# Kernel optimization log

Hardware: AMD Instinct MI355X
Metric: run time of the kernel (lower is better)

Reference implementation:

```python
import jax, jax.numpy as jnp
import numpy as np

NUM_CODES = 512
CODE_DIM = 64
COMMITMENT_COST = 0.1
DECAY = 0.9
EPS = 1e-5


def setup_inputs() -> dict:
    key = jax.random.key(0)
    k1, k2, k3 = jax.random.split(key, 3)
    B, L, D, K = 32, 4096, CODE_DIM, NUM_CODES
    z_e = jax.random.normal(k1, (B, L, D), dtype=jnp.float32)
    emb = jax.random.uniform(k2, (K, D), dtype=jnp.float32, minval=-1.0 / K, maxval=1.0 / K)
    ema_cluster_size = jnp.ones((K,), dtype=jnp.float32)
    ema_w = emb + 0.01 * jax.random.normal(k3, (K, D), dtype=jnp.float32)
    return {"z_e": z_e, "emb": emb, "ema_cluster_size": ema_cluster_size, "ema_w": ema_w}


def reference(z_e, emb, ema_cluster_size, ema_w):
    B, L, D = z_e.shape
    K = emb.shape[0]
    flat = z_e.reshape(-1, D)                                   # [N, D]
    dists = (jnp.sum(flat * flat, axis=1, keepdims=True)
             - 2.0 * flat @ emb.T
             + jnp.sum(emb * emb, axis=1)[None, :])
    codes = jnp.argmin(dists, axis=1)                           # [N] int
    z_q = emb[codes].reshape(B, L, D)
    # straight-through estimator
    z_q_st = z_e + jax.lax.stop_gradient(z_q - z_e)
    # EMA updates (training, no_grad) via direct scatter-reduce instead of one-hot matmul
    cluster_size = jax.ops.segment_sum(jnp.ones_like(codes, dtype=z_e.dtype), codes, num_segments=K)
    new_ecs = ema_cluster_size * DECAY + cluster_size * (1.0 - DECAY)
    dw = jax.ops.segment_sum(flat, codes, num_segments=K)       # [K, D]
    new_ema_w = ema_w * DECAY + dw * (1.0 - DECAY)
    n = jnp.sum(new_ecs)
    cs_smoothed = (new_ecs + EPS) / (n + K * EPS) * n
    new_emb = new_ema_w / (cs_smoothed[:, None] + EPS)
    # commitment loss (z_q detached)
    commit = jnp.mean((z_e - jax.lax.stop_gradient(z_q)) ** 2)
    loss_vq = COMMITMENT_COST * commit
    return (z_q_st, loss_vq, codes.reshape(B, L), new_ecs, new_ema_w, new_emb)
```

## Files before the change

### kernel.cpp

```cpp
#include <hip/hip_runtime.h>
#include <math.h>

#define NROWS 131072
#define DIM 64
#define NCODE 512
#define FLAG_CAP 131072

#define OUT_ZQ    0
#define OUT_LOSS  8388608
#define OUT_CODES 8388609
#define OUT_ECS   8519681
#define OUT_EMAW  8520193
#define OUT_EMB   8552961

#define WS_LOSS    0
#define WS_N       8
#define WS_FLAGC   12
#define WS_COUNTS  16
#define WS_OFFSETS 2064
#define WS_CURSOR  4112
#define WS_CSUM    6160
#define WS_EHI     8208
#define WS_ELO     73744
#define WS_CODESI  139280
#define WS_DW4     139280
#define WS_BUCKET  663568
#define WS_FLAGR   663568
#define WS_BYTES   1187856

#define DECAY_C ((float)0.9)
#define OMD_C   ((float)(1.0 - 0.9))
#define EPS_C   ((float)1e-5)

typedef float f32x4 __attribute__((ext_vector_type(4)));
typedef short short8v __attribute__((ext_vector_type(8)));

__device__ __forceinline__ unsigned short bf16_rne_bits(float f) {
    unsigned int u = __float_as_uint(f);
    unsigned int r = u + 0x7fffu + ((u >> 16) & 1u);
    return (unsigned short)(r >> 16);
}

__device__ __forceinline__ float np_pairwise64_sq(const float* v) {
    float r[8];
#pragma unroll
    for (int j = 0; j < 8; ++j) r[j] = __fmul_rn(v[j], v[j]);
#pragma unroll
    for (int b = 1; b < 8; ++b) {
#pragma unroll
        for (int j = 0; j < 8; ++j)
            r[j] = __fadd_rn(r[j], __fmul_rn(v[8 * b + j], v[8 * b + j]));
    }
    return __fadd_rn(__fadd_rn(__fadd_rn(r[0], r[1]), __fadd_rn(r[2], r[3])),
                     __fadd_rn(__fadd_rn(r[4], r[5]), __fadd_rn(r[6], r[7])));
}

__global__ void k_csum(const float* __restrict__ emb, float* __restrict__ csum,
                       unsigned short* __restrict__ ehi, unsigned short* __restrict__ elo,
                       int* __restrict__ counts, int* __restrict__ flagC,
                       double* __restrict__ lossAcc, float* __restrict__ n_out) {
    int k = blockIdx.x * blockDim.x + threadIdx.x;
    if (k >= NCODE) return;
    counts[k] = 0;
    if (k == 0) { *flagC = 0; *lossAcc = 0.0; *n_out = 0.f; }
    float e[DIM];
#pragma unroll
    for (int d = 0; d < DIM; d += 4) {
        float4 v = *reinterpret_cast<const float4*>(emb + (size_t)k * DIM + d);
        e[d] = v.x; e[d + 1] = v.y; e[d + 2] = v.z; e[d + 3] = v.w;
    }
    csum[k] = np_pairwise64_sq(e);
#pragma unroll
    for (int d = 0; d < DIM; ++d) {
        unsigned short hb = bf16_rne_bits(e[d]);
        float hf = __uint_as_float((unsigned int)hb << 16);
        ehi[k * DIM + d] = hb;
        elo[k * DIM + d] = bf16_rne_bits(e[d] - hf);
    }
}

#define CVTE(H, L, j, val) { \
    unsigned int ub = __float_as_uint(val); \
    unsigned int rr = ub + 0x7fffu + ((ub >> 16) & 1u); \
    unsigned short hb = (unsigned short)(rr >> 16); \
    float hf2 = __uint_as_float(((unsigned int)hb) << 16); \
    float lof = (val) - hf2; \
    unsigned int ul = __float_as_uint(lof); \
    unsigned int rl = ul + 0x7fffu + ((ul >> 16) & 1u); \
    H[j] = (short)hb; L[j] = (short)(rl >> 16); }

__global__ __launch_bounds__(256, 1) void k_mfma(
        const float* __restrict__ ze, const float* __restrict__ emb,
        const unsigned short* __restrict__ ehi, const unsigned short* __restrict__ elo,
        const float* __restrict__ csum, float* __restrict__ out,
        int* __restrict__ codes_i, int* __restrict__ counts,
        double* __restrict__ lossAcc, int* __restrict__ flagC, int* __restrict__ flagR) {
    __shared__ float cs[NCODE];
    __shared__ int h[NCODE];
    __shared__ float A_s[128];
    __shared__ int code_s[128];
    __shared__ double ls[4];
    int tid = threadIdx.x;
    for (int i = tid; i < NCODE; i += 256) { cs[i] = csum[i]; h[i] = 0; }
    if (tid < 128) {
        const float* xr = ze + (size_t)(blockIdx.x * 128 + tid) * DIM;
        float xv[DIM];
#pragma unroll
        for (int d = 0; d < DIM; d += 4) {
            float4 v = *reinterpret_cast<const float4*>(xr + d);
            xv[d] = v.x; xv[d + 1] = v.y; xv[d + 2] = v.z; xv[d + 3] = v.w;
        }
        A_s[tid] = np_pairwise64_sq(xv);
    }
    __syncthreads();

    int wid = tid >> 6;
    int lane = tid & 63;
    int r16 = lane & 15;
    int kg = lane >> 4;
    int rowbase = blockIdx.x * 128 + wid * 32;

    float Ar[2][4];
#pragma unroll
    for (int rt = 0; rt < 2; ++rt)
#pragma unroll
        for (int reg = 0; reg < 4; ++reg)
            Ar[rt][reg] = A_s[wid * 32 + rt * 16 + 4 * kg + reg];

    short8v ahi[2][2], alo[2][2];
#define LOADA(rt, hf) { \
        const float4* ap = reinterpret_cast<const float4*>( \
            ze + (size_t)(rowbase + (rt) * 16 + r16) * DIM + (hf) * 32 + 8 * kg); \
        float4 u = ap[0], w = ap[1]; \
        CVTE(ahi[rt][hf], alo[rt][hf], 0, u.x) CVTE(ahi[rt][hf], alo[rt][hf], 1, u.y) \
        CVTE(ahi[rt][hf], alo[rt][hf], 2, u.z) CVTE(ahi[rt][hf], alo[rt][hf], 3, u.w) \
        CVTE(ahi[rt][hf], alo[rt][hf], 4, w.x) CVTE(ahi[rt][hf], alo[rt][hf], 5, w.y) \
        CVTE(ahi[rt][hf], alo[rt][hf], 6, w.z) CVTE(ahi[rt][hf], alo[rt][hf], 7, w.w) }
    LOADA(0, 0) LOADA(0, 1) LOADA(1, 0) LOADA(1, 1)

    float m1v[2][4], m2v[2][4];
    int i1v[2][4];
#pragma unroll
    for (int rt = 0; rt < 2; ++rt)
#pragma unroll
        for (int j = 0; j < 4; ++j) { m1v[rt][j] = 3.4e38f; m2v[rt][j] = 3.4e38f; i1v[rt][j] = 0; }

#define UPD(C, rt, reg) { \
        float u = __fsub_rn(Ar[rt][reg], __fadd_rn(C[reg], C[reg])); \
        float s = __fadd_rn(u, csv); \
        if (s < m1v[rt][reg]) { m2v[rt][reg] = m1v[rt][reg]; m1v[rt][reg] = s; i1v[rt][reg] = codeIdx; } \
        else if (s < m2v[rt][reg]) { m2v[rt][reg] = s; } }

    for (int t = 0; t < 32; ++t) {
        const short8v* bh = reinterpret_cast<const short8v*>(
            ehi + (size_t)(t * 16 + r16) * DIM + 8 * kg);
        const short8v* bl = reinterpret_cast<const short8v*>(
            elo + (size_t)(t * 16 + r16) * DIM + 8 * kg);
        short8v bh0 = bh[0], bh1 = bh[4];
        short8v bl0 = bl[0], bl1 = bl[4];
        f32x4 c0 = {0.f, 0.f, 0.f, 0.f};
        f32x4 c1 = {0.f, 0.f, 0.f, 0.f};
        c0 = __builtin_amdgcn_mfma_f32_16x16x32_bf16(ahi[0][0], bh0, c0, 0, 0, 0);
        c0 = __builtin_amdgcn_mfma_f32_16x16x32_bf16(ahi[0][1], bh1, c0, 0, 0, 0);
        c0 = __builtin_amdgcn_mfma_f32_16x16x32_bf16(alo[0][0], bh0, c0, 0, 0, 0);
        c0 = __builtin_amdgcn_mfma_f32_16x16x32_bf16(alo[0][1], bh1, c0, 0, 0, 0);
        c0 = __builtin_amdgcn_mfma_f32_16x16x32_bf16(ahi[0][0], bl0, c0, 0, 0, 0);
        c0 = __builtin_amdgcn_mfma_f32_16x16x32_bf16(ahi[0][1], bl1, c0, 0, 0, 0);
        c1 = __builtin_amdgcn_mfma_f32_16x16x32_bf16(ahi[1][0], bh0, c1, 0, 0, 0);
        c1 = __builtin_amdgcn_mfma_f32_16x16x32_bf16(ahi[1][1], bh1, c1, 0, 0, 0);
        c1 = __builtin_amdgcn_mfma_f32_16x16x32_bf16(alo[1][0], bh0, c1, 0, 0, 0);
        c1 = __builtin_amdgcn_mfma_f32_16x16x32_bf16(alo[1][1], bh1, c1, 0, 0, 0);
        c1 = __builtin_amdgcn_mfma_f32_16x16x32_bf16(ahi[1][0], bl0, c1, 0, 0, 0);
        c1 = __builtin_amdgcn_mfma_f32_16x16x32_bf16(ahi[1][1], bl1, c1, 0, 0, 0);
        float csv = cs[t * 16 + r16];
        int codeIdx = t * 16 + r16;
        UPD(c0, 0, 0) UPD(c0, 0, 1) UPD(c0, 0, 2) UPD(c0, 0, 3)
        UPD(c1, 1, 0) UPD(c1, 1, 1) UPD(c1, 1, 2) UPD(c1, 1, 3)
    }

#define RED(rt, reg, mask) { \
        float om1 = __shfl_xor(m1v[rt][reg], mask); \
        int   oi  = __shfl_xor(i1v[rt][reg], mask); \
        float om2 = __shfl_xor(m2v[rt][reg], mask); \
        if (om1 < m1v[rt][reg]) { \
            m2v[rt][reg] = fminf(m1v[rt][reg], om2); m1v[rt][reg] = om1; i1v[rt][reg] = oi; \
        } else if (om1 > m1v[rt][reg]) { \
            m2v[rt][reg] = fminf(m2v[rt][reg], om1); \
        } else { \
            if (oi < i1v[rt][reg]) i1v[rt][reg] = oi; \
            m2v[rt][reg] = m1v[rt][reg]; } }
#define RED4(rt, reg) RED(rt, reg, 1) RED(rt, reg, 2) RED(rt, reg, 4) RED(rt, reg, 8)
    RED4(0, 0) RED4(0, 1) RED4(0, 2) RED4(0, 3)
    RED4(1, 0) RED4(1, 1) RED4(1, 2) RED4(1, 3)

    if (r16 == 0) {
#define WOUT(rt, reg) { \
        int lrow = wid * 32 + (rt) * 16 + 4 * kg + (reg); \
        int row = blockIdx.x * 128 + lrow; \
        code_s[lrow] = i1v[rt][reg]; \
        out[OUT_CODES + row] = (float)i1v[rt][reg]; \
        codes_i[row] = i1v[rt][reg]; \
        atomicAdd(&h[i1v[rt][reg]], 1); \
        if (m2v[rt][reg] - m1v[rt][reg] < Ar[rt][reg] * 3e-7f) { \
            int pos = atomicAdd(flagC, 1); \
            if (pos < FLAG_CAP) flagR[pos] = row; } }
        WOUT(0, 0) WOUT(0, 1) WOUT(0, 2) WOUT(0, 3)
        WOUT(1, 0) WOUT(1, 1) WOUT(1, 2) WOUT(1, 3)
    }
    __syncthreads();

    double lpart = 0.0;
#pragma unroll 4
    for (int r = 0; r < 32; ++r) {
        int code = code_s[wid * 32 + r];
        int row = rowbase + r;
        float x = ze[(size_t)row * DIM + lane];
        float e = emb[(size_t)code * DIM + lane];
        float tdiff = __fsub_rn(e, x);
        out[OUT_ZQ + (size_t)row * DIM + lane] = __fadd_rn(x, tdiff);
        lpart += (double)tdiff * tdiff;
    }
    for (int off = 32; off; off >>= 1) lpart += __shfl_down(lpart, off);
    if (lane == 0) ls[wid] = lpart;
    __syncthreads();
    if (tid == 0) atomicAdd(lossAcc, (ls[0] + ls[1]) + (ls[2] + ls[3]));
    for (int k = tid; k < NCODE; k += 256) {
        int cc = h[k];
        if (cc) atomicAdd(&counts[k], cc);
    }
}

__global__ __launch_bounds__(256) void k_rescue(
        const float* __restrict__ ze, const float* __restrict__ emb,
        const float* __restrict__ csum, float* __restrict__ out,
        int* __restrict__ codes_i, int* __restrict__ counts,
        double* __restrict__ lossAcc, const int* __restrict__ flagC,
        const int* __restrict__ flagR) {
    __shared__ float xs[4][DIM];
    int nf = *flagC;
    if (nf > FLAG_CAP) nf = FLAG_CAP;
    int w = threadIdx.x >> 6;
    int lane = threadIdx.x & 63;
    for (int i = blockIdx.x * 4 + w; i < nf; i += gridDim.x * 4) {
        int row = flagR[i];
        float v = ze[(size_t)row * DIM + lane];
        xs[w][lane] = __fadd_rn(v, v);
        __builtin_amdgcn_wave_barrier();
        float r[8];
#pragma unroll
        for (int j = 0; j < 8; ++j) r[j] = __fmul_rn(xs[w][j], xs[w][j]);
#pragma unroll
        for (int b = 1; b < 8; ++b) {
#pragma unroll
            for (int j = 0; j < 8; ++j)
                r[j] = __fadd_rn(r[j], __fmul_rn(xs[w][8 * b + j], xs[w][8 * b + j]));
        }
        float A = __fmul_rn(0.25f,
            __fadd_rn(__fadd_rn(__fadd_rn(r[0], r[1]), __fadd_rn(r[2], r[3])),
                      __fadd_rn(__fadd_rn(r[4], r[5]), __fadd_rn(r[6], r[7]))));
        float m1 = 3.4e38f;
        int i1 = 0x7fffffff;
#pragma unroll
        for (int kk = 0; kk < 8; ++kk) {
            int k = lane * 8 + kk;
            const float4* e4 = reinterpret_cast<const float4*>(emb + (size_t)k * DIM);
            float a = 0.f;
#pragma unroll
            for (int j = 0; j < 16; ++j) {
                float4 ev = e4[j];
                a = __builtin_fmaf(xs[w][4 * j + 0], ev.x, a);
                a = __builtin_fmaf(xs[w][4 * j + 1], ev.y, a);
                a = __builtin_fmaf(xs[w][4 * j + 2], ev.z, a);
                a = __builtin_fmaf(xs[w][4 * j + 3], ev.w, a);
            }
            float t = __fadd_rn(__fsub_rn(A, a), csum[k]);
            if (t < m1) { m1 = t; i1 = k; }
        }
        for (int off = 32; off; off >>= 1) {
            float ov = __shfl_xor(m1, off);
            int oi = __shfl_xor(i1, off);
            if (ov < m1 || (ov == m1 && oi < i1)) { m1 = ov; i1 = oi; }
        }
        int oldc = codes_i[row];
        if (i1 != oldc) {
            if (lane == 0) {
                codes_i[row] = i1;
                out[OUT_CODES + row] = (float)i1;
                atomicSub(&counts[oldc], 1);
                atomicAdd(&counts[i1], 1);
            }
            float x = __fmul_rn(0.5f, xs[w][lane]);
            float en = emb[(size_t)i1 * DIM + lane];
            float eo = emb[(size_t)oldc * DIM + lane];
            float tn = __fsub_rn(en, x);
            float to = __fsub_rn(eo, x);
            out[OUT_ZQ + (size_t)row * DIM + lane] = __fadd_rn(x, tn);
            double dl = (double)tn * tn - (double)to * to;
            for (int off = 32; off; off >>= 1) dl += __shfl_down(dl, off);
            if (lane == 0) atomicAdd(lossAcc, dl);
        }
        __builtin_amdgcn_wave_barrier();
    }
}

__global__ __launch_bounds__(512) void k_scan(
        const int* __restrict__ counts, int* __restrict__ offsets, int* __restrict__ cursor,
        const float* __restrict__ ecs_in, float* __restrict__ out, float* __restrict__ n_out) {
    __shared__ int sa[NCODE], sb[NCODE];
    __shared__ float red[NCODE];
    int k = threadIdx.x;
    int c = counts[k];
    sa[k] = c;
    float v = __fadd_rn(__fmul_rn(ecs_in[k], DECAY_C), __fmul_rn((float)c, OMD_C));
    out[OUT_ECS + k] = v;
    red[k] = v;
    __syncthreads();
    int* src = sa;
    int* dst = sb;
    for (int off = 1; off < NCODE; off <<= 1) {
        dst[k] = (k >= off) ? src[k - off] + src[k] : src[k];
        __syncthreads();
        int* tp = src; src = dst; dst = tp;
    }
    offsets[k] = src[k] - c;
    cursor[k]  = src[k] - c;
    for (int s = NCODE / 2; s > 0; s >>= 1) {
        if (k < s) red[k] += red[k + s];
        __syncthreads();
    }
    if (k == 0) n_out[0] = red[0];
}

__global__ __launch_bounds__(256) void k_scatter(
        const int* __restrict__ codes_i, int* __restrict__ cursor, int* __restrict__ bucket) {
    int row = blockIdx.x * 256 + threadIdx.x;
    int c = codes_i[row];
    int pos = atomicAdd(&cursor[c], 1);
    bucket[pos] = row;
}

__global__ __launch_bounds__(256) void k_dw(
        const float* __restrict__ ze, const int* __restrict__ bucket,
        const int* __restrict__ offsets, const int* __restrict__ counts,
        float* __restrict__ dw4) {
    __shared__ float p[4][DIM];
    int k = blockIdx.x >> 2;
    int q = blockIdx.x & 3;
    int w = threadIdx.x >> 6;
    int d = threadIdx.x & 63;
    int s = offsets[k];
    int n = counts[k];
    float acc0 = 0.f, acc1 = 0.f;
    int i = q + 4 * w;
    for (; i + 16 < n; i += 32) {
        int ra = bucket[s + i];
        int rb = bucket[s + i + 16];
        acc0 += ze[(size_t)ra * DIM + d];
        acc1 += ze[(size_t)rb * DIM + d];
    }
    if (i < n) acc0 += ze[(size_t)bucket[s + i] * DIM + d];
    p[w][d] = acc0 + acc1;
    __syncthreads();
    if (w == 0) dw4[((size_t)q * NCODE + k) * DIM + d] = (p[0][d] + p[1][d]) + (p[2][d] + p[3][d]);
}

__global__ __launch_bounds__(256) void k_final(
        const float* __restrict__ ema_w, const float* __restrict__ dw4,
        const float* __restrict__ n_ptr, const double* __restrict__ lossAcc,
        float* __restrict__ out) {
    int i = blockIdx.x * blockDim.x + threadIdx.x;
    if (i >= NCODE * DIM) return;
    int k = i >> 6;
    float dsum = __fadd_rn(__fadd_rn(dw4[i], dw4[i + NCODE * DIM]),
                           __fadd_rn(dw4[i + 2 * NCODE * DIM], dw4[i + 3 * NCODE * DIM]));
    float w = __fadd_rn(__fmul_rn(ema_w[i], DECAY_C), __fmul_rn(dsum, OMD_C));
    out[OUT_EMAW + i] = w;
    float n = n_ptr[0];
    float necs = out[OUT_ECS + k];
    float cs = (necs + EPS_C) / (n + (float)NCODE * EPS_C) * n;
    out[OUT_EMB + i] = w / (cs + EPS_C);
    if (i == 0) out[OUT_LOSS] = (float)(0.1 * (lossAcc[0] / (double)((size_t)NROWS * DIM)));
}

extern "C" void kernel_launch(void* const* d_in, const int* in_sizes, int n_in,
                              void* d_out, int out_size, void* d_ws, size_t ws_size,
                              hipStream_t stream) {
    const float* ze   = (const float*)d_in[0];
    const float* emb  = (const float*)d_in[1];
    const float* ecs  = (const float*)d_in[2];
    const float* emaw = (const float*)d_in[3];
    float* out = (float*)d_out;
    char* ws = (char*)d_ws;
    double* lossAcc = (double*)(ws + WS_LOSS);
    float*  n_out   = (float*)(ws + WS_N);
    int*    flagC   = (int*)(ws + WS_FLAGC);
    int*    counts  = (int*)(ws + WS_COUNTS);
    int*    offsets = (int*)(ws + WS_OFFSETS);
    int*    cursor  = (int*)(ws + WS_CURSOR);
    float*  csum    = (float*)(ws + WS_CSUM);
    unsigned short* ehi = (unsigned short*)(ws + WS_EHI);
    unsigned short* elo = (unsigned short*)(ws + WS_ELO);
    int*    codes_i = (int*)(ws + WS_CODESI);
    float*  dw4     = (float*)(ws + WS_DW4);
    int*    bucket  = (int*)(ws + WS_BUCKET);
    int*    flagR   = (int*)(ws + WS_FLAGR);

    hipLaunchKernelGGL(k_csum, dim3(2), dim3(256), 0, stream,
                       emb, csum, ehi, elo, counts, flagC, lossAcc, n_out);
    hipLaunchKernelGGL(k_mfma, dim3(NROWS / 128), dim3(256), 0, stream,
                       ze, emb, ehi, elo, csum, out, codes_i, counts, lossAcc, flagC, flagR);
    hipLaunchKernelGGL(k_rescue, dim3(1024), dim3(256), 0, stream,
                       ze, emb, csum, out, codes_i, counts, lossAcc, flagC, flagR);
    hipLaunchKernelGGL(k_scan, dim3(1), dim3(512), 0, stream,
                       counts, offsets, cursor, ecs, out, n_out);
    hipLaunchKernelGGL(k_scatter, dim3(NROWS / 256), dim3(256), 0, stream,
                       codes_i, cursor, bucket);
    hipLaunchKernelGGL(k_dw, dim3(NCODE * 4), dim3(256), 0, stream,
                       ze, bucket, offsets, counts, dw4);
    hipLaunchKernelGGL(k_final, dim3(NCODE * DIM / 256), dim3(256), 0, stream,
                       emaw, dw4, n_out, lossAcc, out);
}
```

Measured before the change: 208.3 us.

## Split codebook across wave pairs, halve rows per block, merge top-2 via LDS

Result: slower. 225.7 us (+8.4%).

```diff
diff --git a/kernel.cpp b/kernel.cpp
--- a/kernel.cpp
+++ b/kernel.cpp
@@ -97,13 +97,15 @@
         double* __restrict__ lossAcc, int* __restrict__ flagC, int* __restrict__ flagR) {
     __shared__ float cs[NCODE];
     __shared__ int h[NCODE];
-    __shared__ float A_s[128];
-    __shared__ int code_s[128];
+    __shared__ float A_s[64];
+    __shared__ int code_s[64];
+    __shared__ float ms1[64], ms2[64];
+    __shared__ int mi[64];
     __shared__ double ls[4];
     int tid = threadIdx.x;
     for (int i = tid; i < NCODE; i += 256) { cs[i] = csum[i]; h[i] = 0; }
-    if (tid < 128) {
-        const float* xr = ze + (size_t)(blockIdx.x * 128 + tid) * DIM;
+    if (tid < 64) {
+        const float* xr = ze + (size_t)(blockIdx.x * 64 + tid) * DIM;
         float xv[DIM];
 #pragma unroll
         for (int d = 0; d < DIM; d += 4) {
@@ -118,14 +120,16 @@
     int lane = tid & 63;
     int r16 = lane & 15;
     int kg = lane >> 4;
-    int rowbase = blockIdx.x * 128 + wid * 32;
+    int rowgroup = wid & 1;
+    int khalf = __builtin_amdgcn_readfirstlane(wid >> 1);
+    int rowbase = blockIdx.x * 64 + rowgroup * 32;
 
     float Ar[2][4];
 #pragma unroll
     for (int rt = 0; rt < 2; ++rt)
 #pragma unroll
         for (int reg = 0; reg < 4; ++reg)
-            Ar[rt][reg] = A_s[wid * 32 + rt * 16 + 4 * kg + reg];
+            Ar[rt][reg] = A_s[rowgroup * 32 + rt * 16 + 4 * kg + reg];
 
     short8v ahi[2][2], alo[2][2];
 #define LOADA(rt, hf) { \
@@ -151,11 +155,12 @@
         if (s < m1v[rt][reg]) { m2v[rt][reg] = m1v[rt][reg]; m1v[rt][reg] = s; i1v[rt][reg] = codeIdx; } \
         else if (s < m2v[rt][reg]) { m2v[rt][reg] = s; } }
 
-    for (int t = 0; t < 32; ++t) {
+    for (int t = 0; t < 16; ++t) {
+        int codeIdx = (khalf << 8) + t * 16 + r16;
         const short8v* bh = reinterpret_cast<const short8v*>(
-            ehi + (size_t)(t * 16 + r16) * DIM + 8 * kg);
+            ehi + (size_t)codeIdx * DIM + 8 * kg);
         const short8v* bl = reinterpret_cast<const short8v*>(
-            elo + (size_t)(t * 16 + r16) * DIM + 8 * kg);
+            elo + (size_t)codeIdx * DIM + 8 * kg);
         short8v bh0 = bh[0], bh1 = bh[4];
         short8v bl0 = bl[0], bl1 = bl[4];
         f32x4 c0 = {0.f, 0.f, 0.f, 0.f};
@@ -172,8 +177,7 @@
         c1 = __builtin_amdgcn_mfma_f32_16x16x32_bf16(alo[1][1], bh1, c1, 0, 0, 0);
         c1 = __builtin_amdgcn_mfma_f32_16x16x32_bf16(ahi[1][0], bl0, c1, 0, 0, 0);
         c1 = __builtin_amdgcn_mfma_f32_16x16x32_bf16(ahi[1][1], bl1, c1, 0, 0, 0);
-        float csv = cs[t * 16 + r16];
-        int codeIdx = t * 16 + r16;
+        float csv = cs[codeIdx];
         UPD(c0, 0, 0) UPD(c0, 0, 1) UPD(c0, 0, 2) UPD(c0, 0, 3)
         UPD(c1, 1, 0) UPD(c1, 1, 1) UPD(c1, 1, 2) UPD(c1, 1, 3)
     }
@@ -193,15 +197,29 @@
     RED4(0, 0) RED4(0, 1) RED4(0, 2) RED4(0, 3)
     RED4(1, 0) RED4(1, 1) RED4(1, 2) RED4(1, 3)
 
-    if (r16 == 0) {
+    if (khalf == 1 && r16 == 0) {
+#define PUB(rt, reg) { \
+        int lrow = rowgroup * 32 + (rt) * 16 + 4 * kg + (reg); \
+        ms1[lrow] = m1v[rt][reg]; ms2[lrow] = m2v[rt][reg]; mi[lrow] = i1v[rt][reg]; }
+        PUB(0, 0) PUB(0, 1) PUB(0, 2) PUB(0, 3)
+        PUB(1, 0) PUB(1, 1) PUB(1, 2) PUB(1, 3)
+    }
+    __syncthreads();
+
+    if (khalf == 0 && r16 == 0) {
 #define WOUT(rt, reg) { \
-        int lrow = wid * 32 + (rt) * 16 + 4 * kg + (reg); \
-        int row = blockIdx.x * 128 + lrow; \
-        code_s[lrow] = i1v[rt][reg]; \
-        out[OUT_CODES + row] = (float)i1v[rt][reg]; \
-        codes_i[row] = i1v[rt][reg]; \
-        atomicAdd(&h[i1v[rt][reg]], 1); \
-        if (m2v[rt][reg] - m1v[rt][reg] < Ar[rt][reg] * 3e-7f) { \
+        int lrow = rowgroup * 32 + (rt) * 16 + 4 * kg + (reg); \
+        int row = blockIdx.x * 64 + lrow; \
+        float b1 = ms1[lrow], b2 = ms2[lrow]; int bi = mi[lrow]; \
+        float a1 = m1v[rt][reg], a2 = m2v[rt][reg]; int ai = i1v[rt][reg]; \
+        float M1, M2; int I1; \
+        if (b1 < a1) { M1 = b1; I1 = bi; M2 = fminf(a1, b2); } \
+        else         { M1 = a1; I1 = ai; M2 = fminf(a2, b1); } \
+        code_s[lrow] = I1; \
+        out[OUT_CODES + row] = (float)I1; \
+        codes_i[row] = I1; \
+        atomicAdd(&h[I1], 1); \
+        if (M2 - M1 < Ar[rt][reg] * 3e-7f) { \
             int pos = atomicAdd(flagC, 1); \
             if (pos < FLAG_CAP) flagR[pos] = row; } }
         WOUT(0, 0) WOUT(0, 1) WOUT(0, 2) WOUT(0, 3)
@@ -211,9 +229,10 @@
 
     double lpart = 0.0;
 #pragma unroll 4
-    for (int r = 0; r < 32; ++r) {
-        int code = code_s[wid * 32 + r];
-        int row = rowbase + r;
+    for (int r = 0; r < 16; ++r) {
+        int lrow = wid * 16 + r;
+        int code = code_s[lrow];
+        int row = blockIdx.x * 64 + lrow;
         float x = ze[(size_t)row * DIM + lane];
         float e = emb[(size_t)code * DIM + lane];
         float tdiff = __fsub_rn(e, x);
@@ -407,7 +426,7 @@
 
     hipLaunchKernelGGL(k_csum, dim3(2), dim3(256), 0, stream,
                        emb, csum, ehi, elo, counts, flagC, lossAcc, n_out);
-    hipLaunchKernelGGL(k_mfma, dim3(NROWS / 128), dim3(256), 0, stream,
+    hipLaunchKernelGGL(k_mfma, dim3(NROWS / 64), dim3(256), 0, stream,
                        ze, emb, ehi, elo, csum, out, codes_i, counts, lossAcc, flagC, flagR);
     hipLaunchKernelGGL(k_rescue, dim3(1024), dim3(256), 0, stream,
                        ze, emb, csum, out, codes_i, counts, lossAcc, flagC, flagR);
```
